# Performance work log

Hardware: AMD Instinct MI355X
Metric: run time of the kernel (lower is better)

The kernel has to match this reference:

```python
import jax, jax.numpy as jnp
import numpy as np

N, E, IN, H, G = 100000, 1600000, 64, 108, 128
N_LAYERS = 2  # hidden_dims=[108,108] -> 1 layer from hidden_dims[1:] + 1 final layer


def setup_inputs() -> dict:
    key = jax.random.key(0)
    ks = jax.random.split(key, 13)
    s = lambda fan_in: 1.0 / np.sqrt(fan_in)
    inp = {
        "nodes_feat": jax.random.normal(ks[0], (N, IN), jnp.float32),
        "edges_feat": jax.random.normal(ks[1], (E, 1), jnp.float32),
        "nodes_num_norm_sqrt": jax.random.uniform(ks[2], (N,), jnp.float32),
        "edges_num_norm_sqrt": jax.random.uniform(ks[3], (E,), jnp.float32),
        "W_emb": jax.random.uniform(ks[4], (IN, H), jnp.float32, -s(IN), s(IN)),
        "b_emb": jax.random.uniform(ks[5], (H,), jnp.float32, -s(IN), s(IN)),
        "pool_W": jax.random.uniform(ks[6], (N_LAYERS, H, H), jnp.float32, -s(H), s(H)),
        "pool_b": jax.random.uniform(ks[7], (N_LAYERS, H), jnp.float32, -s(H), s(H)),
        "app_W": jax.random.uniform(ks[8], (N_LAYERS, 2 * H, H), jnp.float32, -s(2 * H), s(2 * H)),
        "app_b": jax.random.uniform(ks[9], (N_LAYERS, H), jnp.float32, -s(2 * H), s(2 * H)),
        "src": jax.random.randint(ks[10], (E,), 0, N, jnp.int64 if jax.config.jax_enable_x64 else jnp.int32),
        "dst": jax.random.randint(ks[11], (E,), 0, N, jnp.int64 if jax.config.jax_enable_x64 else jnp.int32),
        "graph_ids": jnp.sort(jax.random.randint(ks[12], (N,), 0, G, jnp.int64 if jax.config.jax_enable_x64 else jnp.int32)),
        "n_graphs": G,
    }
    return inp


def reference(nodes_feat, edges_feat, nodes_num_norm_sqrt, edges_num_norm_sqrt,
              W_emb, b_emb, pool_W, pool_b, app_W, app_b,
              src, dst, graph_ids, n_graphs):
    n = nodes_feat.shape[0]
    # embedding_h
    h = nodes_feat @ W_emb + b_emb  # [N, H]
    # in-degree for mean aggregation (dropout = 0.0 so omitted)
    deg = jax.ops.segment_sum(jnp.ones((src.shape[0],), h.dtype), dst, num_segments=n)
    deg = jnp.maximum(deg, 1.0)[:, None]  # [N, 1]
    for i in range(pool_W.shape[0]):
        h_in = h
        # meanpool aggregator: per-message linear+ReLU == per-node transform then gather
        z = jax.nn.relu(h @ pool_W[i] + pool_b[i])  # [N, H]
        c = jax.ops.segment_sum(z[src], dst, num_segments=n) / deg  # mean over neighbors
        # NodeApply: linear(concat(h, c)) -> L2 normalize -> activation
        b = jnp.concatenate([h, c], axis=1) @ app_W[i] + app_b[i]
        b = b / jnp.maximum(jnp.linalg.norm(b, axis=1, keepdims=True), 1e-12)
        h = h_in + jax.nn.relu(b)  # residual (dims match: 108 == 108)
    # dgl.mean_nodes readout per graph
    cnt = jax.ops.segment_sum(jnp.ones((n,), h.dtype), graph_ids, num_segments=n_graphs)
    hg = jax.ops.segment_sum(h, graph_ids, num_segments=n_graphs) / jnp.maximum(cnt, 1.0)[:, None]
    return hg  # [n_graphs, H]
```

## Files before the change

kernel.cpp:

```cpp
#include <hip/hip_runtime.h>

#define HDIM 108
constexpr int G_GRAPHS = 128;
constexpr int MAXNB = 1024;
constexpr int CAP = 2560;

typedef _Float16 half8 __attribute__((ext_vector_type(8)));
typedef _Float16 half4v __attribute__((ext_vector_type(4)));
typedef float floatx4 __attribute__((ext_vector_type(4)));
typedef float floatx2 __attribute__((ext_vector_type(2)));

__device__ inline unsigned char f32_to_fp8(float t) {
#if __has_builtin(__builtin_amdgcn_cvt_pk_fp8_f32)
  return (unsigned char)(__builtin_amdgcn_cvt_pk_fp8_f32(t, t, 0, false) & 0xFF);
#else
  t = fminf(t, 448.f);
  if (t < 0.015625f) return (unsigned char)__float2int_rn(t * 512.f);
  unsigned u = __float_as_uint(t);
  unsigned lsb = (u >> 20) & 1;
  u += 0x7FFFFu + lsb;
  int e = (int)((u >> 23) & 0xFF) - 127;
  if (e > 8) return 0x7E;
  return (unsigned char)(((e + 7) << 3) | ((u >> 20) & 7));
#endif
}

template <bool HI>
__device__ inline floatx2 fp8x2_to_f32(unsigned v) {
#if __has_builtin(__builtin_amdgcn_cvt_pk_f32_fp8)
  return __builtin_amdgcn_cvt_pk_f32_fp8((int)v, HI);
#else
  unsigned b0 = HI ? ((v >> 16) & 0xFF) : (v & 0xFF);
  unsigned b1 = HI ? ((v >> 24) & 0xFF) : ((v >> 8) & 0xFF);
  floatx2 r;
  {
    unsigned s = b0 >> 7, e = (b0 >> 3) & 0xF, m = b0 & 7;
    float f = (e == 0) ? (float)m * 0.001953125f
                       : __uint_as_float(((e + 120u) << 23) | (m << 20));
    r[0] = s ? -f : f;
  }
  {
    unsigned s = b1 >> 7, e = (b1 >> 3) & 0xF, m = b1 & 7;
    float f = (e == 0) ? (float)m * 0.001953125f
                       : __uint_as_float(((e + 120u) << 23) | (m << 20));
    r[1] = s ? -f : f;
  }
  return r;
#endif
}

__global__ __launch_bounds__(256) void k_cvtall(const float* __restrict__ W_emb,
                                                const float* __restrict__ pool_W,
                                                const float* __restrict__ app_W,
                                                _Float16* __restrict__ wte,
                                                _Float16* __restrict__ wtp,
                                                _Float16* __restrict__ wta) {
  int idx = blockIdx.x * 256 + threadIdx.x;
  if (idx >= 86016) return;
  const float* src;
  _Float16* dst;
  int Kpad, K, split, rel;
  if (idx < 7168)       { rel = idx;          src = W_emb;            dst = wte;              Kpad = 64;  K = 64;  split = 0; }
  else if (idx < 21504) { rel = idx - 7168;   src = pool_W;           dst = wtp;              Kpad = 128; K = 108; split = 0; }
  else if (idx < 35840) { rel = idx - 21504;  src = pool_W + 11664;   dst = wtp + 14336;      Kpad = 128; K = 108; split = 0; }
  else if (idx < 60928) { rel = idx - 35840;  src = app_W;            dst = wta;              Kpad = 224; K = 216; split = 1; }
  else                  { rel = idx - 60928;  src = app_W + 23328;    dst = wta + 25088;      Kpad = 224; K = 216; split = 1; }
  int n = rel / Kpad, k = rel - n * Kpad;
  int ks;
  if (split) ks = (k < 108) ? k : (k >= 112 && k < 220) ? (k - 4) : -1;
  else       ks = (k < K) ? k : -1;
  float v = (n < 108 && ks >= 0) ? src[ks * 108 + n] : 0.f;
  dst[rel] = (_Float16)v;
}

__global__ __launch_bounds__(1024) void k_scatter(const int* __restrict__ src, const int* __restrict__ dst,
                                                  int* __restrict__ gcur, int* __restrict__ ebuf,
                                                  int E, int nb) {
  __shared__ int hist[MAXNB];
  const int tid = threadIdx.x;
  const int e0 = blockIdx.x * 16384;
  for (int b = tid; b < nb; b += 1024) hist[b] = 0;
  __syncthreads();
#pragma unroll
  for (int it = 0; it < 16; it++) {
    int e = e0 + it * 1024 + tid;
    if (e < E) atomicAdd(&hist[dst[e] >> 7], 1);
  }
  __syncthreads();
  for (int b = tid; b < nb; b += 1024) {
    int h = hist[b];
    hist[b] = h ? atomicAdd(&gcur[b * 16], h) : 0;
  }
  __syncthreads();
#pragma unroll
  for (int it = 0; it < 16; it++) {
    int e = e0 + it * 1024 + tid;
    if (e < E) {
      int d = dst[e];
      int b = d >> 7;
      int rank = atomicAdd(&hist[b], 1);
      if (rank < CAP) ebuf[(size_t)b * CAP + rank] = src[e] | ((d & 127) << 20);
    }
  }
}

__global__ __launch_bounds__(1024) void k_bagg(const unsigned char* __restrict__ z, const int* __restrict__ ebuf,
                                               const int* __restrict__ gcur, _Float16* __restrict__ c16,
                                               int N, int nb) {
  __shared__ int cnts[128];
  __shared__ int scanb[128];
  __shared__ int off[129];
  __shared__ int ecur[128];
  __shared__ int esrc[CAP];
  const int tid = threadIdx.x;
  const int b = blockIdx.x;
  const int v0 = b << 7;
  int cntb = gcur[b * 16];
  if (cntb > CAP) cntb = CAP;
  const int* eb = ebuf + (size_t)b * CAP;

  if (tid < 128) cnts[tid] = 0;
  __syncthreads();
  for (int i = tid; i < cntb; i += 1024) atomicAdd(&cnts[eb[i] >> 20], 1);
  __syncthreads();
  if (tid < 128) scanb[tid] = cnts[tid];
  __syncthreads();
#pragma unroll
  for (int st = 1; st < 128; st <<= 1) {
    int v = 0;
    if (tid < 128 && tid >= st) v = scanb[tid - st];
    __syncthreads();
    if (tid < 128) scanb[tid] += v;
    __syncthreads();
  }
  if (tid == 0) off[0] = 0;
  if (tid < 128) {
    off[tid + 1] = scanb[tid];
    ecur[tid] = scanb[tid] - cnts[tid];
  }
  __syncthreads();
  for (int i = tid; i < cntb; i += 1024) {
    int e = eb[i];
    int p = atomicAdd(&ecur[e >> 20], 1);
    esrc[p] = e & 0xFFFFF;
  }
  __syncthreads();

  const int lane = tid & 31;
  const int grp = tid >> 5;
  if (lane >= 28) return;
  const unsigned char* __restrict__ zl = z + lane * 4;
#pragma unroll 1
  for (int r = grp; r < 128; r += 32) {
    int v = v0 + r;
    if (v >= N) continue;
    int s = off[r], e2 = off[r + 1];
    float a0 = 0.f, a1 = 0.f, a2 = 0.f, a3 = 0.f;
    int j = s;
    for (; j + 4 <= e2; j += 4) {
      unsigned q0 = *(const unsigned*)(zl + (size_t)esrc[j] * 112);
      unsigned q1 = *(const unsigned*)(zl + (size_t)esrc[j + 1] * 112);
      unsigned q2 = *(const unsigned*)(zl + (size_t)esrc[j + 2] * 112);
      unsigned q3 = *(const unsigned*)(zl + (size_t)esrc[j + 3] * 112);
      floatx2 l0 = fp8x2_to_f32<false>(q0), h0 = fp8x2_to_f32<true>(q0);
      floatx2 l1 = fp8x2_to_f32<false>(q1), h1 = fp8x2_to_f32<true>(q1);
      floatx2 l2 = fp8x2_to_f32<false>(q2), h2 = fp8x2_to_f32<true>(q2);
      floatx2 l3 = fp8x2_to_f32<false>(q3), h3 = fp8x2_to_f32<true>(q3);
      a0 += (l0[0] + l1[0]) + (l2[0] + l3[0]);
      a1 += (l0[1] + l1[1]) + (l2[1] + l3[1]);
      a2 += (h0[0] + h1[0]) + (h2[0] + h3[0]);
      a3 += (h0[1] + h1[1]) + (h2[1] + h3[1]);
    }
    for (; j < e2; j++) {
      unsigned q0 = *(const unsigned*)(zl + (size_t)esrc[j] * 112);
      floatx2 l0 = fp8x2_to_f32<false>(q0), h0 = fp8x2_to_f32<true>(q0);
      a0 += l0[0]; a1 += l0[1]; a2 += h0[0]; a3 += h0[1];
    }
    int d = e2 - s;
    float inv = 1.f / (float)(d > 0 ? d : 1);
    half4v r4;
    r4[0] = (_Float16)(a0 * inv); r4[1] = (_Float16)(a1 * inv);
    r4[2] = (_Float16)(a2 * inv); r4[3] = (_Float16)(a3 * inv);
    *(half4v*)(c16 + (size_t)v * 112 + lane * 4) = r4;
  }
}

template <int KCH, int MODE>
__global__ __launch_bounds__(256, 2) void k_mmf(const void* Asrc, const _Float16* __restrict__ c16,
                                                const _Float16* __restrict__ Wt, const float* __restrict__ bias,
                                                void* outp, int N) {
  constexpr int KW = KCH * 32;
  __shared__ _Float16 As[128 * 40];
  __shared__ _Float16 Ws[112 * 40];

  const int tid = threadIdx.x;
  const int wave = tid >> 6;
  const int lane = tid & 63;
  const int lo = lane & 15;
  const int quad = lane >> 4;
  const int n0 = blockIdx.x * 128;
  const _Float16* h16 = (const _Float16*)Asrc;
  const float* feat = (const float*)Asrc;

  floatx4 acc[2][7];
#pragma unroll
  for (int rt = 0; rt < 2; rt++)
#pragma unroll
    for (int ct = 0; ct < 7; ct++) {
      floatx4 zz = {0.f, 0.f, 0.f, 0.f};
      acc[rt][ct] = zz;
    }

#pragma unroll 1
  for (int kc = 0; kc < KCH; kc++) {
#pragma unroll
    for (int it = 0; it < 2; it++) {
      int idx = tid + it * 256;
      int r = idx >> 2, sg = idx & 3;
      int gn = n0 + r;
      int k = kc * 32 + sg * 8;
      half8 v = {0, 0, 0, 0, 0, 0, 0, 0};
      if (gn < N) {
        if (MODE == 0) {
          float4 f0 = *(const float4*)(feat + (size_t)gn * 64 + k);
          float4 f1 = *(const float4*)(feat + (size_t)gn * 64 + k + 4);
          v[0] = (_Float16)f0.x; v[1] = (_Float16)f0.y; v[2] = (_Float16)f0.z; v[3] = (_Float16)f0.w;
          v[4] = (_Float16)f1.x; v[5] = (_Float16)f1.y; v[6] = (_Float16)f1.z; v[7] = (_Float16)f1.w;
        } else if (MODE == 2) {
          const _Float16* sp = (k < 112) ? (h16 + (size_t)gn * 112 + k)
                                         : (c16 + (size_t)gn * 112 + (k - 112));
          v = *(const half8*)sp;
        } else {
          if (k < 112) v = *(const half8*)(h16 + (size_t)gn * 112 + k);
        }
      }
      *(half8*)&As[r * 40 + sg * 8] = v;
    }
#pragma unroll
    for (int it = 0; it < 2; it++) {
      int idx = tid + it * 256;
      if (idx < 112 * 4) {
        int nrow = idx >> 2, sg = idx & 3;
        half8 v = *(const half8*)(Wt + (size_t)nrow * KW + kc * 32 + sg * 8);
        *(half8*)&Ws[nrow * 40 + sg * 8] = v;
      }
    }
    __syncthreads();

    half8 a0 = *(const half8*)&As[(wave * 32 + lo) * 40 + quad * 8];
    half8 a1 = *(const half8*)&As[(wave * 32 + 16 + lo) * 40 + quad * 8];
#pragma unroll
    for (int ct = 0; ct < 7; ct++) {
      half8 b = *(const half8*)&Ws[(ct * 16 + lo) * 40 + quad * 8];
      acc[0][ct] = __builtin_amdgcn_mfma_f32_16x16x32_f16(a0, b, acc[0][ct], 0, 0, 0);
      acc[1][ct] = __builtin_amdgcn_mfma_f32_16x16x32_f16(a1, b, acc[1][ct], 0, 0, 0);
    }
    __syncthreads();
  }

  float bias_v[7];
#pragma unroll
  for (int ct = 0; ct < 7; ct++) {
    int col = ct * 16 + lo;
    bias_v[ct] = (col < 108) ? bias[col] : 0.f;
  }

  if (MODE == 2) {
    _Float16* out16 = (_Float16*)outp;
#pragma unroll
    for (int rt = 0; rt < 2; rt++) {
#pragma unroll
      for (int reg = 0; reg < 4; reg++) {
        int gr = n0 + wave * 32 + rt * 16 + quad * 4 + reg;
        float bv[7];
        float ssq = 0.f;
#pragma unroll
        for (int ct = 0; ct < 7; ct++) {
          float t = acc[rt][ct][reg] + bias_v[ct];
          bv[ct] = t;
          ssq += t * t;
        }
#pragma unroll
        for (int s = 1; s < 16; s <<= 1) ssq += __shfl_xor(ssq, s, 16);
        float scale = 1.f / fmaxf(sqrtf(ssq), 1e-12f);
        if (gr < N) {
          _Float16* hp = out16 + (size_t)gr * 112 + lo;
#pragma unroll
          for (int ct = 0; ct < 7; ct++) {
            float hv = (float)hp[ct * 16];
            hp[ct * 16] = (_Float16)(hv + fmaxf(bv[ct] * scale, 0.f));
          }
        }
      }
    }
  } else if (MODE == 1) {
    unsigned char* outb = (unsigned char*)outp;
#pragma unroll
    for (int rt = 0; rt < 2; rt++) {
#pragma unroll
      for (int reg = 0; reg < 4; reg++) {
        int gr = n0 + wave * 32 + rt * 16 + quad * 4 + reg;
        if (gr < N) {
          unsigned char* op = outb + (size_t)gr * 112 + lo;
#pragma unroll
          for (int ct = 0; ct < 7; ct++) {
            float t = fmaxf(acc[rt][ct][reg] + bias_v[ct], 0.f);
            op[ct * 16] = f32_to_fp8(t);
          }
        }
      }
    }
  } else {
    _Float16* out16 = (_Float16*)outp;
#pragma unroll
    for (int rt = 0; rt < 2; rt++) {
#pragma unroll
      for (int reg = 0; reg < 4; reg++) {
        int gr = n0 + wave * 32 + rt * 16 + quad * 4 + reg;
        if (gr < N) {
          _Float16* op = out16 + (size_t)gr * 112 + lo;
#pragma unroll
          for (int ct = 0; ct < 7; ct++) {
            float t = acc[rt][ct][reg] + bias_v[ct];
            op[ct * 16] = (_Float16)t;
          }
        }
      }
    }
  }
}

__global__ __launch_bounds__(256) void k_readout(const _Float16* __restrict__ h, const int* __restrict__ gid,
                                                 float* __restrict__ hg, int N) {
  const int CH = 64;
  const int lane = threadIdx.x & 31;
  const int grp = threadIdx.x >> 5;
  int start = (blockIdx.x * 8 + grp) * CH;
  if (start >= N || lane >= 27) return;
  int end = min(start + CH, N);
  float a0 = 0.f, a1 = 0.f, a2 = 0.f, a3 = 0.f;
  int cur = gid[start];
  for (int i = start; i < end; i++) {
    int g = gid[i];
    if (g != cur) {
      float* base = &hg[(size_t)cur * HDIM + lane * 4];
      atomicAdd(base + 0, a0); atomicAdd(base + 1, a1);
      atomicAdd(base + 2, a2); atomicAdd(base + 3, a3);
      a0 = a1 = a2 = a3 = 0.f;
      cur = g;
    }
    half4v v = *(const half4v*)(h + (size_t)i * 112 + lane * 4);
    a0 += (float)v[0]; a1 += (float)v[1]; a2 += (float)v[2]; a3 += (float)v[3];
  }
  float* base = &hg[(size_t)cur * HDIM + lane * 4];
  atomicAdd(base + 0, a0); atomicAdd(base + 1, a1);
  atomicAdd(base + 2, a2); atomicAdd(base + 3, a3);
}

__global__ __launch_bounds__(256) void k_div(const float* __restrict__ hg, const int* __restrict__ gid,
                                             float* __restrict__ out, int total, int N) {
  int i = blockIdx.x * 256 + threadIdx.x;
  if (i < total) {
    int g = i / HDIM;
    int lo = 0, hi = N;
    while (lo < hi) { int m = (lo + hi) >> 1; if (gid[m] < g) lo = m + 1; else hi = m; }
    int lb = lo;
    lo = 0; hi = N;
    while (lo < hi) { int m = (lo + hi) >> 1; if (gid[m] <= g) lo = m + 1; else hi = m; }
    int c = lo - lb;
    out[i] = hg[i] / (float)(c > 0 ? c : 1);
  }
}

extern "C" void kernel_launch(void* const* d_in, const int* in_sizes, int n_in,
                              void* d_out, int out_size, void* d_ws, size_t ws_size,
                              hipStream_t stream) {
  (void)n_in; (void)ws_size; (void)out_size;
  const float* nodes_feat = (const float*)d_in[0];
  const float* W_emb = (const float*)d_in[4];
  const float* b_emb = (const float*)d_in[5];
  const float* pool_W = (const float*)d_in[6];
  const float* pool_b = (const float*)d_in[7];
  const float* app_W = (const float*)d_in[8];
  const float* app_b = (const float*)d_in[9];
  const int* src = (const int*)d_in[10];
  const int* dst = (const int*)d_in[11];
  const int* gid = (const int*)d_in[12];
  const int N = in_sizes[2];
  const int E = in_sizes[10];
  float* out = (float*)d_out;

  const int nb = (N + 127) >> 7;

  char* ws = (char*)d_ws;
  size_t off = 0;
  auto alloc = [&](size_t bytes) -> size_t {
    size_t o = off;
    off += (bytes + 1023) & ~size_t(1023);
    return o;
  };
  size_t o_gcur = alloc((size_t)MAXNB * 16 * 4);
  size_t o_hg   = alloc((size_t)G_GRAPHS * HDIM * 4);
  size_t zero_bytes = off;
  size_t o_ebuf = alloc((size_t)MAXNB * CAP * 4);
  size_t o_h  = alloc((size_t)N * 112 * 2);
  size_t o_z  = alloc((size_t)N * 112);
  size_t o_c  = alloc((size_t)N * 112 * 2);
  size_t o_we = alloc((size_t)112 * 64 * 2);
  size_t o_wp = alloc((size_t)2 * 112 * 128 * 2);
  size_t o_wa = alloc((size_t)2 * 112 * 224 * 2);

  int*           gcur = (int*)(ws + o_gcur);
  float*         hg   = (float*)(ws + o_hg);
  int*           ebuf = (int*)(ws + o_ebuf);
  _Float16*      h16  = (_Float16*)(ws + o_h);
  unsigned char* z8   = (unsigned char*)(ws + o_z);
  _Float16*      c16  = (_Float16*)(ws + o_c);
  _Float16*      wte  = (_Float16*)(ws + o_we);
  _Float16*      wtp  = (_Float16*)(ws + o_wp);
  _Float16*      wta  = (_Float16*)(ws + o_wa);

  (void)hipMemsetAsync(d_ws, 0, zero_bytes, stream);

  k_cvtall<<<(86016 + 255) / 256, 256, 0, stream>>>(W_emb, pool_W, app_W, wte, wtp, wta);

  k_scatter<<<(E + 16383) / 16384, 1024, 0, stream>>>(src, dst, gcur, ebuf, E, nb);

  const int nbMM = (N + 127) / 128;
  k_mmf<2, 0><<<nbMM, 256, 0, stream>>>(nodes_feat, nullptr, wte, b_emb, h16, N);

  for (int i = 0; i < 2; i++) {
    k_mmf<4, 1><<<nbMM, 256, 0, stream>>>(h16, nullptr, wtp + i * 112 * 128,
                                          pool_b + i * HDIM, z8, N);
    k_bagg<<<nb, 1024, 0, stream>>>(z8, ebuf, gcur, c16, N, nb);
    k_mmf<7, 2><<<nbMM, 256, 0, stream>>>(h16, c16, wta + i * 112 * 224,
                                          app_b + i * HDIM, h16, N);
  }

  k_readout<<<(N + 8 * 64 - 1) / (8 * 64), 256, 0, stream>>>(h16, gid, hg, N);
  k_div<<<(G_GRAPHS * HDIM + 255) / 256, 256, 0, stream>>>(hg, gid, out, G_GRAPHS * HDIM, N);
}
```

Measured before the change: 348.6 us.

## Fuse pool transform into preceding matmul and readout into final apply

Each node-apply (and the embedding) matmul now keeps the new h tile in shared memory and immediately runs the next layer's pool linear+ReLU on it, writing fp8 z directly. The last apply kernel does the per-graph readout from shared memory instead of writing h. Weight conversion is folded into the scatter kernel, and the z row stride goes from 112 to 128 bytes. This removes several launches and a round-trip of h through global memory, at the cost of extra shared memory per block, which may lower occupancy.

```diff
diff --git a/kernel.cpp b/kernel.cpp
--- a/kernel.cpp
+++ b/kernel.cpp
@@ -49,36 +49,37 @@
 #endif
 }
 
-__global__ __launch_bounds__(256) void k_cvtall(const float* __restrict__ W_emb,
-                                                const float* __restrict__ pool_W,
-                                                const float* __restrict__ app_W,
-                                                _Float16* __restrict__ wte,
-                                                _Float16* __restrict__ wtp,
-                                                _Float16* __restrict__ wta) {
-  int idx = blockIdx.x * 256 + threadIdx.x;
-  if (idx >= 86016) return;
-  const float* src;
-  _Float16* dst;
-  int Kpad, K, split, rel;
-  if (idx < 7168)       { rel = idx;          src = W_emb;            dst = wte;              Kpad = 64;  K = 64;  split = 0; }
-  else if (idx < 21504) { rel = idx - 7168;   src = pool_W;           dst = wtp;              Kpad = 128; K = 108; split = 0; }
-  else if (idx < 35840) { rel = idx - 21504;  src = pool_W + 11664;   dst = wtp + 14336;      Kpad = 128; K = 108; split = 0; }
-  else if (idx < 60928) { rel = idx - 35840;  src = app_W;            dst = wta;              Kpad = 224; K = 216; split = 1; }
-  else                  { rel = idx - 60928;  src = app_W + 23328;    dst = wta + 25088;      Kpad = 224; K = 216; split = 1; }
-  int n = rel / Kpad, k = rel - n * Kpad;
-  int ks;
-  if (split) ks = (k < 108) ? k : (k >= 112 && k < 220) ? (k - 4) : -1;
-  else       ks = (k < K) ? k : -1;
-  float v = (n < 108 && ks >= 0) ? src[ks * 108 + n] : 0.f;
-  dst[rel] = (_Float16)v;
-}
-
 __global__ __launch_bounds__(1024) void k_scatter(const int* __restrict__ src, const int* __restrict__ dst,
                                                   int* __restrict__ gcur, int* __restrict__ ebuf,
+                                                  const float* __restrict__ W_emb,
+                                                  const float* __restrict__ pool_W,
+                                                  const float* __restrict__ app_W,
+                                                  _Float16* __restrict__ wte,
+                                                  _Float16* __restrict__ wtp,
+                                                  _Float16* __restrict__ wta,
                                                   int E, int nb) {
   __shared__ int hist[MAXNB];
   const int tid = threadIdx.x;
   const int e0 = blockIdx.x * 16384;
+
+  int gi = blockIdx.x * 1024 + tid;
+  if (gi < 86016) {
+    const float* srcw;
+    _Float16* dstw;
+    int Kpad, K, split, rel;
+    if (gi < 7168)       { rel = gi;          srcw = W_emb;          dstw = wte;         Kpad = 64;  K = 64;  split = 0; }
+    else if (gi < 21504) { rel = gi - 7168;   srcw = pool_W;         dstw = wtp;         Kpad = 128; K = 108; split = 0; }
+    else if (gi < 35840) { rel = gi - 21504;  srcw = pool_W + 11664; dstw = wtp + 14336; Kpad = 128; K = 108; split = 0; }
+    else if (gi < 60928) { rel = gi - 35840;  srcw = app_W;          dstw = wta;         Kpad = 224; K = 216; split = 1; }
+    else                 { rel = gi - 60928;  srcw = app_W + 23328;  dstw = wta + 25088; Kpad = 224; K = 216; split = 1; }
+    int n = rel / Kpad, k = rel - n * Kpad;
+    int ks;
+    if (split) ks = (k < 108) ? k : (k >= 112 && k < 220) ? (k - 4) : -1;
+    else       ks = (k < K) ? k : -1;
+    float v = (n < 108 && ks >= 0) ? srcw[ks * 108 + n] : 0.f;
+    dstw[rel] = (_Float16)v;
+  }
+
   for (int b = tid; b < nb; b += 1024) hist[b] = 0;
   __syncthreads();
 #pragma unroll
@@ -158,10 +159,10 @@
     float a0 = 0.f, a1 = 0.f, a2 = 0.f, a3 = 0.f;
     int j = s;
     for (; j + 4 <= e2; j += 4) {
-      unsigned q0 = *(const unsigned*)(zl + (size_t)esrc[j] * 112);
-      unsigned q1 = *(const unsigned*)(zl + (size_t)esrc[j + 1] * 112);
-      unsigned q2 = *(const unsigned*)(zl + (size_t)esrc[j + 2] * 112);
-      unsigned q3 = *(const unsigned*)(zl + (size_t)esrc[j + 3] * 112);
+      unsigned q0 = *(const unsigned*)(zl + (size_t)esrc[j] * 128);
+      unsigned q1 = *(const unsigned*)(zl + (size_t)esrc[j + 1] * 128);
+      unsigned q2 = *(const unsigned*)(zl + (size_t)esrc[j + 2] * 128);
+      unsigned q3 = *(const unsigned*)(zl + (size_t)esrc[j + 3] * 128);
       floatx2 l0 = fp8x2_to_f32<false>(q0), h0 = fp8x2_to_f32<true>(q0);
       floatx2 l1 = fp8x2_to_f32<false>(q1), h1 = fp8x2_to_f32<true>(q1);
       floatx2 l2 = fp8x2_to_f32<false>(q2), h2 = fp8x2_to_f32<true>(q2);
@@ -172,7 +173,7 @@
       a3 += (h0[1] + h1[1]) + (h2[1] + h3[1]);
     }
     for (; j < e2; j++) {
-      unsigned q0 = *(const unsigned*)(zl + (size_t)esrc[j] * 112);
+      unsigned q0 = *(const unsigned*)(zl + (size_t)esrc[j] * 128);
       floatx2 l0 = fp8x2_to_f32<false>(q0), h0 = fp8x2_to_f32<true>(q0);
       a0 += l0[0]; a1 += l0[1]; a2 += h0[0]; a3 += h0[1];
     }
@@ -185,13 +186,17 @@
   }
 }
 
-template <int KCH, int MODE>
+template <int KCH, int MODE, bool POOL>
 __global__ __launch_bounds__(256, 2) void k_mmf(const void* Asrc, const _Float16* __restrict__ c16,
                                                 const _Float16* __restrict__ Wt, const float* __restrict__ bias,
-                                                void* outp, int N) {
+                                                const _Float16* __restrict__ Wtp, const float* __restrict__ bias_p,
+                                                _Float16* __restrict__ outh, unsigned char* __restrict__ outz,
+                                                const int* __restrict__ gid, float* __restrict__ hg, int N) {
   constexpr int KW = KCH * 32;
+  constexpr int HST = POOL ? 136 : 120;
   __shared__ _Float16 As[128 * 40];
   __shared__ _Float16 Ws[112 * 40];
+  __shared__ _Float16 hL[128 * HST];
 
   const int tid = threadIdx.x;
   const int wave = tid >> 6;
@@ -201,6 +206,13 @@
   const int n0 = blockIdx.x * 128;
   const _Float16* h16 = (const _Float16*)Asrc;
   const float* feat = (const float*)Asrc;
+
+  if (POOL) {
+    for (int i = tid; i < 128 * 16; i += 256) {
+      int r = i >> 4, cc = i & 15;
+      hL[r * HST + 112 + cc] = (_Float16)0;
+    }
+  }
 
   floatx4 acc[2][7];
 #pragma unroll
@@ -226,12 +238,10 @@
           float4 f1 = *(const float4*)(feat + (size_t)gn * 64 + k + 4);
           v[0] = (_Float16)f0.x; v[1] = (_Float16)f0.y; v[2] = (_Float16)f0.z; v[3] = (_Float16)f0.w;
           v[4] = (_Float16)f1.x; v[5] = (_Float16)f1.y; v[6] = (_Float16)f1.z; v[7] = (_Float16)f1.w;
-        } else if (MODE == 2) {
+        } else {
           const _Float16* sp = (k < 112) ? (h16 + (size_t)gn * 112 + k)
                                          : (c16 + (size_t)gn * 112 + (k - 112));
           v = *(const half8*)sp;
-        } else {
-          if (k < 112) v = *(const half8*)(h16 + (size_t)gn * 112 + k);
         }
       }
       *(half8*)&As[r * 40 + sg * 8] = v;
@@ -265,13 +275,28 @@
     bias_v[ct] = (col < 108) ? bias[col] : 0.f;
   }
 
-  if (MODE == 2) {
-    _Float16* out16 = (_Float16*)outp;
+  if (MODE == 0) {
 #pragma unroll
     for (int rt = 0; rt < 2; rt++) {
 #pragma unroll
       for (int reg = 0; reg < 4; reg++) {
-        int gr = n0 + wave * 32 + rt * 16 + quad * 4 + reg;
+        int rl = wave * 32 + rt * 16 + quad * 4 + reg;
+        int gr = n0 + rl;
+#pragma unroll
+        for (int ct = 0; ct < 7; ct++) {
+          float t = acc[rt][ct][reg] + bias_v[ct];
+          hL[rl * HST + ct * 16 + lo] = (_Float16)t;
+          if (gr < N) outh[(size_t)gr * 112 + ct * 16 + lo] = (_Float16)t;
+        }
+      }
+    }
+  } else {
+#pragma unroll
+    for (int rt = 0; rt < 2; rt++) {
+#pragma unroll
+      for (int reg = 0; reg < 4; reg++) {
+        int rl = wave * 32 + rt * 16 + quad * 4 + reg;
+        int gr = n0 + rl;
         float bv[7];
         float ssq = 0.f;
 #pragma unroll
@@ -283,78 +308,95 @@
 #pragma unroll
         for (int s = 1; s < 16; s <<= 1) ssq += __shfl_xor(ssq, s, 16);
         float scale = 1.f / fmaxf(sqrtf(ssq), 1e-12f);
-        if (gr < N) {
-          _Float16* hp = out16 + (size_t)gr * 112 + lo;
-#pragma unroll
-          for (int ct = 0; ct < 7; ct++) {
-            float hv = (float)hp[ct * 16];
-            hp[ct * 16] = (_Float16)(hv + fmaxf(bv[ct] * scale, 0.f));
-          }
-        }
-      }
-    }
-  } else if (MODE == 1) {
-    unsigned char* outb = (unsigned char*)outp;
+#pragma unroll
+        for (int ct = 0; ct < 7; ct++) {
+          float hv = (gr < N) ? (float)h16[(size_t)gr * 112 + ct * 16 + lo] : 0.f;
+          float t = hv + fmaxf(bv[ct] * scale, 0.f);
+          hL[rl * HST + ct * 16 + lo] = (_Float16)t;
+          if (MODE == 2 && gr < N) outh[(size_t)gr * 112 + ct * 16 + lo] = (_Float16)t;
+        }
+      }
+    }
+  }
+  __syncthreads();
+
+  if (POOL) {
+#pragma unroll
+    for (int rt = 0; rt < 2; rt++)
+#pragma unroll
+      for (int ct = 0; ct < 7; ct++) {
+        floatx4 zz = {0.f, 0.f, 0.f, 0.f};
+        acc[rt][ct] = zz;
+      }
+#pragma unroll 1
+    for (int kc = 0; kc < 4; kc++) {
+#pragma unroll
+      for (int it = 0; it < 2; it++) {
+        int idx = tid + it * 256;
+        if (idx < 112 * 4) {
+          int nrow = idx >> 2, sg = idx & 3;
+          half8 v = *(const half8*)(Wtp + (size_t)nrow * 128 + kc * 32 + sg * 8);
+          *(half8*)&Ws[nrow * 40 + sg * 8] = v;
+        }
+      }
+      __syncthreads();
+      half8 a0 = *(const half8*)&hL[(wave * 32 + lo) * HST + kc * 32 + quad * 8];
+      half8 a1 = *(const half8*)&hL[(wave * 32 + 16 + lo) * HST + kc * 32 + quad * 8];
+#pragma unroll
+      for (int ct = 0; ct < 7; ct++) {
+        half8 b = *(const half8*)&Ws[(ct * 16 + lo) * 40 + quad * 8];
+        acc[0][ct] = __builtin_amdgcn_mfma_f32_16x16x32_f16(a0, b, acc[0][ct], 0, 0, 0);
+        acc[1][ct] = __builtin_amdgcn_mfma_f32_16x16x32_f16(a1, b, acc[1][ct], 0, 0, 0);
+      }
+      __syncthreads();
+    }
+    float bp_v[7];
+#pragma unroll
+    for (int ct = 0; ct < 7; ct++) {
+      int col = ct * 16 + lo;
+      bp_v[ct] = (col < 108) ? bias_p[col] : 0.f;
+    }
 #pragma unroll
     for (int rt = 0; rt < 2; rt++) {
 #pragma unroll
       for (int reg = 0; reg < 4; reg++) {
         int gr = n0 + wave * 32 + rt * 16 + quad * 4 + reg;
         if (gr < N) {
-          unsigned char* op = outb + (size_t)gr * 112 + lo;
+          unsigned char* op = outz + (size_t)gr * 128 + lo;
 #pragma unroll
           for (int ct = 0; ct < 7; ct++) {
-            float t = fmaxf(acc[rt][ct][reg] + bias_v[ct], 0.f);
+            float t = fmaxf(acc[rt][ct][reg] + bp_v[ct], 0.f);
             op[ct * 16] = f32_to_fp8(t);
           }
         }
       }
     }
-  } else {
-    _Float16* out16 = (_Float16*)outp;
-#pragma unroll
-    for (int rt = 0; rt < 2; rt++) {
-#pragma unroll
-      for (int reg = 0; reg < 4; reg++) {
-        int gr = n0 + wave * 32 + rt * 16 + quad * 4 + reg;
-        if (gr < N) {
-          _Float16* op = out16 + (size_t)gr * 112 + lo;
-#pragma unroll
-          for (int ct = 0; ct < 7; ct++) {
-            float t = acc[rt][ct][reg] + bias_v[ct];
-            op[ct * 16] = (_Float16)t;
-          }
-        }
-      }
-    }
-  }
-}
-
-__global__ __launch_bounds__(256) void k_readout(const _Float16* __restrict__ h, const int* __restrict__ gid,
-                                                 float* __restrict__ hg, int N) {
-  const int CH = 64;
-  const int lane = threadIdx.x & 31;
-  const int grp = threadIdx.x >> 5;
-  int start = (blockIdx.x * 8 + grp) * CH;
-  if (start >= N || lane >= 27) return;
-  int end = min(start + CH, N);
-  float a0 = 0.f, a1 = 0.f, a2 = 0.f, a3 = 0.f;
-  int cur = gid[start];
-  for (int i = start; i < end; i++) {
-    int g = gid[i];
-    if (g != cur) {
-      float* base = &hg[(size_t)cur * HDIM + lane * 4];
+  } else if (MODE == 3) {
+    const int lane31 = tid & 31;
+    const int grp8 = tid >> 5;
+    int r0 = grp8 * 16;
+    if (lane31 < 27 && n0 + r0 < N) {
+      float a0 = 0.f, a1 = 0.f, a2 = 0.f, a3 = 0.f;
+      int cur = gid[n0 + r0];
+      for (int r = r0; r < r0 + 16; r++) {
+        int gn = n0 + r;
+        if (gn >= N) break;
+        int g = gid[gn];
+        if (g != cur) {
+          float* base = &hg[(size_t)cur * HDIM + lane31 * 4];
+          atomicAdd(base + 0, a0); atomicAdd(base + 1, a1);
+          atomicAdd(base + 2, a2); atomicAdd(base + 3, a3);
+          a0 = a1 = a2 = a3 = 0.f;
+          cur = g;
+        }
+        half4v v = *(const half4v*)&hL[r * HST + lane31 * 4];
+        a0 += (float)v[0]; a1 += (float)v[1]; a2 += (float)v[2]; a3 += (float)v[3];
+      }
+      float* base = &hg[(size_t)cur * HDIM + lane31 * 4];
       atomicAdd(base + 0, a0); atomicAdd(base + 1, a1);
       atomicAdd(base + 2, a2); atomicAdd(base + 3, a3);
-      a0 = a1 = a2 = a3 = 0.f;
-      cur = g;
-    }
-    half4v v = *(const half4v*)(h + (size_t)i * 112 + lane * 4);
-    a0 += (float)v[0]; a1 += (float)v[1]; a2 += (float)v[2]; a3 += (float)v[3];
-  }
-  float* base = &hg[(size_t)cur * HDIM + lane * 4];
-  atomicAdd(base + 0, a0); atomicAdd(base + 1, a1);
-  atomicAdd(base + 2, a2); atomicAdd(base + 3, a3);
+    }
+  }
 }
 
 __global__ __launch_bounds__(256) void k_div(const float* __restrict__ hg, const int* __restrict__ gid,
@@ -404,7 +446,7 @@
   size_t zero_bytes = off;
   size_t o_ebuf = alloc((size_t)MAXNB * CAP * 4);
   size_t o_h  = alloc((size_t)N * 112 * 2);
-  size_t o_z  = alloc((size_t)N * 112);
+  size_t o_z  = alloc((size_t)N * 128);
   size_t o_c  = alloc((size_t)N * 112 * 2);
   size_t o_we = alloc((size_t)112 * 64 * 2);
   size_t o_wp = alloc((size_t)2 * 112 * 128 * 2);
@@ -422,21 +464,19 @@
 
   (void)hipMemsetAsync(d_ws, 0, zero_bytes, stream);
 
-  k_cvtall<<<(86016 + 255) / 256, 256, 0, stream>>>(W_emb, pool_W, app_W, wte, wtp, wta);
-
-  k_scatter<<<(E + 16383) / 16384, 1024, 0, stream>>>(src, dst, gcur, ebuf, E, nb);
+  k_scatter<<<(E + 16383) / 16384, 1024, 0, stream>>>(src, dst, gcur, ebuf,
+                                                      W_emb, pool_W, app_W,
+                                                      wte, wtp, wta, E, nb);
 
   const int nbMM = (N + 127) / 128;
-  k_mmf<2, 0><<<nbMM, 256, 0, stream>>>(nodes_feat, nullptr, wte, b_emb, h16, N);
-
-  for (int i = 0; i < 2; i++) {
-    k_mmf<4, 1><<<nbMM, 256, 0, stream>>>(h16, nullptr, wtp + i * 112 * 128,
-                                          pool_b + i * HDIM, z8, N);
-    k_bagg<<<nb, 1024, 0, stream>>>(z8, ebuf, gcur, c16, N, nb);
-    k_mmf<7, 2><<<nbMM, 256, 0, stream>>>(h16, c16, wta + i * 112 * 224,
-                                          app_b + i * HDIM, h16, N);
-  }
-
-  k_readout<<<(N + 8 * 64 - 1) / (8 * 64), 256, 0, stream>>>(h16, gid, hg, N);
+  k_mmf<2, 0, true><<<nbMM, 256, 0, stream>>>(nodes_feat, nullptr, wte, b_emb,
+                                              wtp, pool_b, h16, z8, nullptr, nullptr, N);
+  k_bagg<<<nb, 1024, 0, stream>>>(z8, ebuf, gcur, c16, N, nb);
+  k_mmf<7, 2, true><<<nbMM, 256, 0, stream>>>(h16, c16, wta, app_b,
+                                              wtp + 14336, pool_b + HDIM, h16, z8, nullptr, nullptr, N);
+  k_bagg<<<nb, 1024, 0, stream>>>(z8, ebuf, gcur, c16, N, nb);
+  k_mmf<7, 3, false><<<nbMM, 256, 0, stream>>>(h16, c16, wta + 25088, app_b + HDIM,
+                                               nullptr, nullptr, nullptr, nullptr, gid, hg, N);
+
   k_div<<<(G_GRAPHS * HDIM + 255) / 256, 256, 0, stream>>>(hg, gid, out, G_GRAPHS * HDIM, N);
 }
```

Measured after the change: 365.2 us. 1.05x slower.
